# Kernel optimization log

Measured on AMD Instinct MI355X. Metric: run time of the kernel, lower is better.

## Reference

```python
import jax, jax.numpy as jnp
import numpy as np

NUM_HEADS = 16
ROPE_SEGMENTS = (1024, 512)  # remainder of the sequence is left un-roped
ROPE_THETA = 10000.0
EPS = 1e-6


def _rmsnorm(t, w):
    # t: [B,H,N,D]; norm over last dim in fp32, then scale
    tf = t.astype(jnp.float32)
    n = tf * jax.lax.rsqrt(jnp.mean(tf * tf, axis=-1, keepdims=True) + EPS)
    return n.astype(t.dtype) * w


def _rope(t):
    # t: [B,H,S,D]; positions restart at 0 for each call (segment-local RoPE)
    S, D = t.shape[-2], t.shape[-1]
    inv_freq = 1.0 / (ROPE_THETA ** (jnp.arange(0, D, 2, dtype=jnp.float32) / D))  # [D/2]
    ang = jnp.arange(S, dtype=jnp.float32)[:, None] * inv_freq[None, :]            # [S,D/2]
    cos, sin = jnp.cos(ang), jnp.sin(ang)
    t1, t2 = t[..., : D // 2], t[..., D // 2 :]
    return jnp.concatenate([t1 * cos - t2 * sin, t2 * cos + t1 * sin], axis=-1).astype(t.dtype)


def _segmented_rope(t, N):
    parts, start = [], 0
    for seg in ROPE_SEGMENTS:
        parts.append(_rope(t[:, :, start : start + seg, :]))
        start += seg
    if start < N:
        parts.append(t[:, :, start:, :])
    return jnp.concatenate(parts, axis=2)


def setup_inputs() -> dict:
    key = jax.random.key(0)
    ks = jax.random.split(key, 5)
    B, N, C = 2, 2048, 1024
    D = C // NUM_HEADS
    s = 1.0 / np.sqrt(C)
    return {
        "x": jax.random.normal(ks[0], (B, N, C), jnp.float32),
        "qkv_w": jax.random.normal(ks[1], (3 * C, C), jnp.float32) * s,
        "qkv_b": jax.random.normal(ks[2], (3 * C,), jnp.float32) * 0.02,
        "qn_w": jnp.ones((D,), jnp.float32),
        "kn_w": jnp.ones((D,), jnp.float32),
        "proj_w": jax.random.normal(ks[3], (C, C), jnp.float32) * s,
        "proj_b": jax.random.normal(ks[4], (C,), jnp.float32) * 0.02,
    }


def reference(x, qkv_w, qkv_b, qn_w, kn_w, proj_w, proj_b):
    B, N, C = x.shape
    H = NUM_HEADS
    D = C // H
    qkv = (x @ qkv_w.T + qkv_b).reshape(B, N, 3, H, D)
    qkv = jnp.transpose(qkv, (2, 0, 3, 1, 4))  # [3,B,H,N,D]
    q, k, v = qkv[0], qkv[1], qkv[2]
    q = _rmsnorm(q, qn_w)
    k = _rmsnorm(k, kn_w)
    q = _segmented_rope(q, N)
    k = _segmented_rope(k, N)
    scale = 1.0 / np.sqrt(D)  # SDPA default scale
    scores = jnp.einsum("bhqd,bhkd->bhqk", q, k) * scale
    attn = jax.nn.softmax(scores, axis=-1)
    out = jnp.einsum("bhqk,bhkd->bhqd", attn, v)           # [B,H,N,D]
    out = jnp.transpose(out, (0, 2, 1, 3)).reshape(B, N, C)
    return out @ proj_w.T + proj_b
```

## Files before the change

kernel.cpp:

```cpp
#include <hip/hip_runtime.h>

typedef __attribute__((ext_vector_type(8))) short short8;
typedef __attribute__((ext_vector_type(4))) float f32x4;

__device__ __forceinline__ float bf2f(unsigned short u) {
    union { unsigned int i; float f; } c; c.i = ((unsigned int)u) << 16; return c.f;
}
__device__ __forceinline__ unsigned short f2bf(float f) {
    union { float f; unsigned int i; } c; c.f = f;
    unsigned int u = c.i;
    return (unsigned short)((u + 0x7fffu + ((u >> 16) & 1u)) >> 16);
}

__device__ __forceinline__ void glds16(const void* g, void* l) {
    __builtin_amdgcn_global_load_lds(
        (const __attribute__((address_space(1))) unsigned int*)g,
        (__attribute__((address_space(3))) unsigned int*)l, 16, 0, 0);
}

__global__ __launch_bounds__(256) void prep(
    const float* __restrict__ x, const float* __restrict__ qkv_w,
    const float* __restrict__ proj_w,
    const float* __restrict__ qn_w, const float* __restrict__ kn_w,
    unsigned short* __restrict__ xb, unsigned short* __restrict__ qwb,
    unsigned short* __restrict__ pwb, float* __restrict__ mb2)
{
    const int b = blockIdx.x, tid = threadIdx.x;
    const float* src; unsigned short* dst; int i;
    if (b < 4096)      { src = x;      dst = xb;  i = b * 256 + tid; }
    else if (b < 7168) { src = qkv_w;  dst = qwb; i = (b - 4096) * 256 + tid; }
    else if (b < 8192) { src = proj_w; dst = pwb; i = (b - 7168) * 256 + tid; }
    else {
        if (tid < 64) {
            float a = fabsf(qn_w[tid]), bb = fabsf(kn_w[tid]);
#pragma unroll
            for (int off = 32; off; off >>= 1) {
                a = fmaxf(a, __shfl_xor(a, off));
                bb = fmaxf(bb, __shfl_xor(bb, off));
            }
            if (tid == 0) *mb2 = 8.0f * a * bb * 1.4426950408889634f;
        }
        return;
    }
    float4 v = ((const float4*)src)[i];
    ushort4 o;
    o.x = f2bf(v.x); o.y = f2bf(v.y); o.z = f2bf(v.z); o.w = f2bf(v.w);
    ((ushort4*)dst)[i] = o;
}

__global__ __launch_bounds__(256) void gemm_qkv(
    const unsigned short* __restrict__ A,
    const unsigned short* __restrict__ W,
    const float* __restrict__ bias,
    const float* __restrict__ qn_w, const float* __restrict__ kn_w,
    unsigned short* __restrict__ qb, unsigned short* __restrict__ kb,
    unsigned short* __restrict__ vt)
{
    __shared__ unsigned short As[128 * 32];
    __shared__ unsigned short Ws[128 * 32];
    const int tid = threadIdx.x;
    const int w = tid >> 6, l = tid & 63, quad = l >> 4, low = l & 15;
    const int m0 = blockIdx.y * 128, n0 = blockIdx.x * 128;
    const int wm = w >> 1, wn = w & 1;
    const int K = 1024;

    f32x4 acc[4][4];
#pragma unroll
    for (int i = 0; i < 4; i++)
#pragma unroll
        for (int j = 0; j < 4; j++) acc[i][j] = (f32x4){0.f, 0.f, 0.f, 0.f};

    const int r1 = tid >> 2, p1 = tid & 3;
    const int c1 = p1 ^ ((r1 >> 1) & 3);
    const int r2 = r1 + 64;
    const int c2 = p1 ^ ((r2 >> 1) & 3);
    const unsigned short* ga1 = A + (size_t)(m0 + r1) * K + c1 * 8;
    const unsigned short* ga2 = A + (size_t)(m0 + r2) * K + c2 * 8;
    const unsigned short* gw1 = W + (size_t)(n0 + r1) * K + c1 * 8;
    const unsigned short* gw2 = W + (size_t)(n0 + r2) * K + c2 * 8;
    char* lA = (char*)As + (w << 10);
    char* lW = (char*)Ws + (w << 10);

    for (int k0 = 0; k0 < K; k0 += 32) {
        __syncthreads();
        glds16(ga1 + k0, lA);
        glds16(ga2 + k0, lA + 4096);
        glds16(gw1 + k0, lW);
        glds16(gw2 + k0, lW + 4096);
        __syncthreads();
        short8 af[4], wf[4];
#pragma unroll
        for (int i = 0; i < 4; i++) {
            const int ra = wm * 64 + i * 16 + low;
            af[i] = *(const short8*)&As[ra * 32 + (quad ^ ((ra >> 1) & 3)) * 8];
            const int rw = wn * 64 + i * 16 + low;
            wf[i] = *(const short8*)&Ws[rw * 32 + (quad ^ ((rw >> 1) & 3)) * 8];
        }
#pragma unroll
        for (int i = 0; i < 4; i++)
#pragma unroll
            for (int j = 0; j < 4; j++)
                acc[i][j] = __builtin_amdgcn_mfma_f32_16x16x32_bf16(
                    af[i], wf[j], acc[i][j], 0, 0, 0);
    }

    const int colbase = n0 + wn * 64;
    const int t3 = colbase >> 10;
    const int hh = (colbase & 1023) >> 6;
    float wv4[4] = {0, 0, 0, 0}, invA = 0.f, invB = 0.f;
    if (t3 < 2) {
        const float* nw = (t3 == 0) ? qn_w : kn_w;
#pragma unroll
        for (int j = 0; j < 4; j++) wv4[j] = nw[j * 16 + low];
        const float c0 = -2.0f * 13.287712379549449f / 64.0f;
        invA = exp2f(c0 * (float)low);
        invB = exp2f(c0 * (float)(16 + low));
    }
    unsigned short* dqk = (t3 == 0) ? qb : kb;

#pragma unroll
    for (int i = 0; i < 4; i++) {
#pragma unroll
        for (int reg = 0; reg < 4; reg++) {
            const int gm = m0 + wm * 64 + i * 16 + quad * 4 + reg;
            const int b_ = gm >> 11, npos = gm & 2047;
            float v[4];
#pragma unroll
            for (int j = 0; j < 4; j++)
                v[j] = acc[i][j][reg] + bias[colbase + j * 16 + low];
            if (t3 == 2) {
#pragma unroll
                for (int j = 0; j < 4; j++)
                    vt[((size_t)(b_ * 16 + hh) * 64 + j * 16 + low) * 2048 + npos] =
                        f2bf(v[j]);
            } else {
                float ss = v[0]*v[0] + v[1]*v[1] + v[2]*v[2] + v[3]*v[3];
                ss += __shfl_xor(ss, 1); ss += __shfl_xor(ss, 2);
                ss += __shfl_xor(ss, 4); ss += __shfl_xor(ss, 8);
                const float r = rsqrtf(ss * (1.0f / 64.0f) + 1e-6f);
                float nv[4];
#pragma unroll
                for (int j = 0; j < 4; j++) nv[j] = v[j] * r * wv4[j];
                float o0, o1, o2, o3;
                if (npos < 1536) {
                    const float p = (float)((npos < 1024) ? npos : (npos - 1024));
                    float sA, cA, sB, cB;
                    __sincosf(p * invA, &sA, &cA);
                    __sincosf(p * invB, &sB, &cB);
                    o0 = nv[0] * cA - nv[2] * sA;
                    o1 = nv[1] * cB - nv[3] * sB;
                    o2 = nv[2] * cA + nv[0] * sA;
                    o3 = nv[3] * cB + nv[1] * sB;
                } else { o0 = nv[0]; o1 = nv[1]; o2 = nv[2]; o3 = nv[3]; }
                unsigned short* drow =
                    dqk + ((size_t)(b_ * 16 + hh) * 2048 + npos) * 64 + low;
                drow[0]  = f2bf(o0);
                drow[16] = f2bf(o1);
                drow[32] = f2bf(o2);
                drow[48] = f2bf(o3);
            }
        }
    }
}

__global__ __launch_bounds__(256) void flash_mfma(
    const unsigned short* __restrict__ qg, const unsigned short* __restrict__ kg,
    const unsigned short* __restrict__ vg, unsigned short* __restrict__ ao,
    const float* __restrict__ mb2p)
{
    __shared__ unsigned short Ks[64 * 64];
    __shared__ unsigned short Vs[64 * 64];
    __shared__ unsigned short Ps[4][16 * 72];

    const int tid = threadIdx.x;
    const int w = tid >> 6, l = tid & 63, quad = l >> 4, low = l & 15;
    const int bh = blockIdx.y, q0 = blockIdx.x * 64;
    const float MB2 = *mb2p;
    const float SCL = 0.125f * 1.4426950408889634f;

    short8 qa[2];
#pragma unroll
    for (int kh = 0; kh < 2; kh++) {
        const int qrow = q0 + w * 16 + low;
        qa[kh] = *(const short8*)(qg + ((size_t)bh * 2048 + qrow) * 64 +
                                  kh * 32 + quad * 8);
    }

    f32x4 o[4], lsum = (f32x4){0.f, 0.f, 0.f, 0.f};
#pragma unroll
    for (int db = 0; db < 4; db++) o[db] = (f32x4){0.f, 0.f, 0.f, 0.f};
    short8 ones;
#pragma unroll
    for (int j = 0; j < 8; j++) ones[j] = (short)0x3F80;

    const int kr1 = tid >> 3, kp1 = tid & 7, kc1 = kp1 ^ (kr1 & 7);
    const int kr2 = kr1 + 32, kc2 = kp1 ^ (kr2 & 7);
    const unsigned short* gk1 = kg + ((size_t)bh * 2048 + kr1) * 64 + kc1 * 8;
    const unsigned short* gk2 = kg + ((size_t)bh * 2048 + kr2) * 64 + kc2 * 8;
    const unsigned short* gv1 = vg + ((size_t)bh * 64 + kr1) * 2048 + kc1 * 8;
    const unsigned short* gv2 = vg + ((size_t)bh * 64 + kr2) * 2048 + kc2 * 8;
    char* lK = (char*)Ks + (w << 10);
    char* lV = (char*)Vs + (w << 10);
    unsigned short* myP = Ps[w];

    for (int kt = 0; kt < 32; kt++) {
        const size_t ko = (size_t)kt * 4096;
        const int vo = kt * 64;
        __syncthreads();
        glds16(gk1 + ko, lK);
        glds16(gk2 + ko, lK + 4096);
        glds16(gv1 + vo, lV);
        glds16(gv2 + vo, lV + 4096);
        __syncthreads();

#pragma unroll
        for (int kb = 0; kb < 4; kb++) {
            const int krow = kb * 16 + low;
            const short8 kf0 = *(const short8*)&Ks[krow * 64 + (quad ^ (krow & 7)) * 8];
            const short8 kf1 = *(const short8*)&Ks[krow * 64 + ((4 + quad) ^ (krow & 7)) * 8];
            f32x4 s = __builtin_amdgcn_mfma_f32_16x16x32_bf16(
                kf0, qa[0], (f32x4){0.f, 0.f, 0.f, 0.f}, 0, 0, 0);
            s = __builtin_amdgcn_mfma_f32_16x16x32_bf16(kf1, qa[1], s, 0, 0, 0);
            unsigned int pb[4];
#pragma unroll
            for (int reg = 0; reg < 4; reg++) {
                union { float f; unsigned int u; } cc;
                cc.f = exp2f(fmaf(s[reg], SCL, -MB2));
                pb[reg] = cc.u;
            }
            const unsigned int u0 = __builtin_amdgcn_perm(pb[1], pb[0], 0x07060302u);
            const unsigned int u1 = __builtin_amdgcn_perm(pb[3], pb[2], 0x07060302u);
            *(uint2*)&myP[low * 72 + kb * 16 + quad * 4] = make_uint2(u0, u1);
        }

        short8 pa[2];
#pragma unroll
        for (int kh = 0; kh < 2; kh++)
            pa[kh] = *(const short8*)&myP[low * 72 + kh * 32 + quad * 8];
        lsum = __builtin_amdgcn_mfma_f32_16x16x32_bf16(pa[0], ones, lsum, 0, 0, 0);
        lsum = __builtin_amdgcn_mfma_f32_16x16x32_bf16(pa[1], ones, lsum, 0, 0, 0);
#pragma unroll
        for (int db = 0; db < 4; db++) {
            const int d = db * 16 + low;
            const short8 vf0 = *(const short8*)&Vs[d * 64 + (quad ^ (d & 7)) * 8];
            const short8 vf1 = *(const short8*)&Vs[d * 64 + ((4 + quad) ^ (d & 7)) * 8];
            o[db] = __builtin_amdgcn_mfma_f32_16x16x32_bf16(pa[0], vf0, o[db], 0, 0, 0);
            o[db] = __builtin_amdgcn_mfma_f32_16x16x32_bf16(pa[1], vf1, o[db], 0, 0, 0);
        }
    }

    const int b_ = bh >> 4, h = bh & 15;
    float inv[4];
#pragma unroll
    for (int reg = 0; reg < 4; reg++) inv[reg] = 1.0f / lsum[reg];
#pragma unroll
    for (int db = 0; db < 4; db++)
#pragma unroll
        for (int reg = 0; reg < 4; reg++) {
            const int n = q0 + w * 16 + quad * 4 + reg;
            ao[((size_t)(b_ * 2048 + n)) * 1024 + h * 64 + db * 16 + low] =
                f2bf(o[db][reg] * inv[reg]);
        }
}

__global__ __launch_bounds__(256) void gemm_out(
    const unsigned short* __restrict__ A,
    const unsigned short* __restrict__ W,
    const float* __restrict__ bias,
    float* __restrict__ outp)
{
    __shared__ unsigned short As[64 * 32];
    __shared__ unsigned short Ws[128 * 32];
    const int tid = threadIdx.x;
    const int w = tid >> 6, l = tid & 63, quad = l >> 4, low = l & 15;
    const int m0 = blockIdx.y * 64, n0 = blockIdx.x * 128;
    const int wm = w >> 1, wn = w & 1;
    const int K = 1024;

    f32x4 acc[2][4];
#pragma unroll
    for (int i = 0; i < 2; i++)
#pragma unroll
        for (int j = 0; j < 4; j++) acc[i][j] = (f32x4){0.f, 0.f, 0.f, 0.f};

    const int r1 = tid >> 2, p1 = tid & 3;
    const int c1 = p1 ^ ((r1 >> 1) & 3);
    const int r2 = r1 + 64;
    const int c2 = p1 ^ ((r2 >> 1) & 3);
    const unsigned short* ga = A + (size_t)(m0 + r1) * K + c1 * 8;
    const unsigned short* gw1 = W + (size_t)(n0 + r1) * K + c1 * 8;
    const unsigned short* gw2 = W + (size_t)(n0 + r2) * K + c2 * 8;
    char* lA = (char*)As + (w << 10);
    char* lW = (char*)Ws + (w << 10);

    for (int k0 = 0; k0 < K; k0 += 32) {
        __syncthreads();
        glds16(ga + k0, lA);
        glds16(gw1 + k0, lW);
        glds16(gw2 + k0, lW + 4096);
        __syncthreads();
        short8 af[2], wf[4];
#pragma unroll
        for (int i = 0; i < 2; i++) {
            const int ra = wm * 32 + i * 16 + low;
            af[i] = *(const short8*)&As[ra * 32 + (quad ^ ((ra >> 1) & 3)) * 8];
        }
#pragma unroll
        for (int j = 0; j < 4; j++) {
            const int rw = wn * 64 + j * 16 + low;
            wf[j] = *(const short8*)&Ws[rw * 32 + (quad ^ ((rw >> 1) & 3)) * 8];
        }
#pragma unroll
        for (int i = 0; i < 2; i++)
#pragma unroll
            for (int j = 0; j < 4; j++)
                acc[i][j] = __builtin_amdgcn_mfma_f32_16x16x32_bf16(
                    af[i], wf[j], acc[i][j], 0, 0, 0);
    }

#pragma unroll
    for (int i = 0; i < 2; i++)
#pragma unroll
        for (int j = 0; j < 4; j++) {
            const int gc = n0 + wn * 64 + j * 16 + low;
            const float bv = bias[gc];
#pragma unroll
            for (int reg = 0; reg < 4; reg++) {
                const int gm = m0 + wm * 32 + i * 16 + quad * 4 + reg;
                outp[(size_t)gm * 1024 + gc] = acc[i][j][reg] + bv;
            }
        }
}

extern "C" void kernel_launch(void* const* d_in, const int* in_sizes, int n_in,
                              void* d_out, int out_size, void* d_ws, size_t ws_size,
                              hipStream_t stream)
{
    const float* x      = (const float*)d_in[0];
    const float* qkv_w  = (const float*)d_in[1];
    const float* qkv_b  = (const float*)d_in[2];
    const float* qn_w   = (const float*)d_in[3];
    const float* kn_w   = (const float*)d_in[4];
    const float* proj_w = (const float*)d_in[5];
    const float* proj_b = (const float*)d_in[6];

    char* base = (char*)d_ws;
    float* mb2          = (float*)base;
    unsigned short* xb  = (unsigned short*)(base + 256);
    unsigned short* qwb = xb  + 4194304;
    unsigned short* pwb = qwb + 3145728;
    unsigned short* qb  = pwb + 1048576;
    unsigned short* kb  = qb  + 4194304;
    unsigned short* vt  = kb  + 4194304;
    unsigned short* ao  = vt  + 4194304;

    prep<<<8193, 256, 0, stream>>>(x, qkv_w, proj_w, qn_w, kn_w, xb, qwb, pwb, mb2);

    gemm_qkv<<<dim3(24, 32), 256, 0, stream>>>(xb, qwb, qkv_b, qn_w, kn_w,
                                               qb, kb, vt);

    flash_mfma<<<dim3(32, 32), 256, 0, stream>>>(qb, kb, vt, ao, mb2);

    gemm_out<<<dim3(8, 64), 256, 0, stream>>>(ao, pwb, proj_b, (float*)d_out);
}
```

Before: 216.2 us.

## Use 32x32 MFMA in flash attention and stage V transpose through LDS

```diff
diff --git a/kernel.cpp b/kernel.cpp
--- a/kernel.cpp
+++ b/kernel.cpp
@@ -2,6 +2,7 @@
 
 typedef __attribute__((ext_vector_type(8))) short short8;
 typedef __attribute__((ext_vector_type(4))) float f32x4;
+typedef __attribute__((ext_vector_type(16))) float f32x16;
 
 __device__ __forceinline__ float bf2f(unsigned short u) {
     union { unsigned int i; float f; } c; c.i = ((unsigned int)u) << 16; return c.f;
@@ -17,6 +18,8 @@
         (const __attribute__((address_space(1))) unsigned int*)g,
         (__attribute__((address_space(3))) unsigned int*)l, 16, 0, 0);
 }
+
+union i4s8 { int4 i; short8 s; };
 
 __global__ __launch_bounds__(256) void prep(
     const float* __restrict__ x, const float* __restrict__ qkv_w,
@@ -56,8 +59,7 @@
     unsigned short* __restrict__ qb, unsigned short* __restrict__ kb,
     unsigned short* __restrict__ vt)
 {
-    __shared__ unsigned short As[128 * 32];
-    __shared__ unsigned short Ws[128 * 32];
+    __shared__ unsigned short pool[128 * 136];
     const int tid = threadIdx.x;
     const int w = tid >> 6, l = tid & 63, quad = l >> 4, low = l & 15;
     const int m0 = blockIdx.y * 128, n0 = blockIdx.x * 128;
@@ -78,8 +80,8 @@
     const unsigned short* ga2 = A + (size_t)(m0 + r2) * K + c2 * 8;
     const unsigned short* gw1 = W + (size_t)(n0 + r1) * K + c1 * 8;
     const unsigned short* gw2 = W + (size_t)(n0 + r2) * K + c2 * 8;
-    char* lA = (char*)As + (w << 10);
-    char* lW = (char*)Ws + (w << 10);
+    char* lA = (char*)pool + (w << 10);
+    char* lW = (char*)pool + 8192 + (w << 10);
 
     for (int k0 = 0; k0 < K; k0 += 32) {
         __syncthreads();
@@ -92,9 +94,9 @@
 #pragma unroll
         for (int i = 0; i < 4; i++) {
             const int ra = wm * 64 + i * 16 + low;
-            af[i] = *(const short8*)&As[ra * 32 + (quad ^ ((ra >> 1) & 3)) * 8];
+            af[i] = *(const short8*)&pool[ra * 32 + (quad ^ ((ra >> 1) & 3)) * 8];
             const int rw = wn * 64 + i * 16 + low;
-            wf[i] = *(const short8*)&Ws[rw * 32 + (quad ^ ((rw >> 1) & 3)) * 8];
+            wf[i] = *(const short8*)&pool[4096 + rw * 32 + (quad ^ ((rw >> 1) & 3)) * 8];
         }
 #pragma unroll
         for (int i = 0; i < 4; i++)
@@ -105,17 +107,44 @@
     }
 
     const int colbase = n0 + wn * 64;
-    const int t3 = colbase >> 10;
+    const int t3 = n0 >> 10;
     const int hh = (colbase & 1023) >> 6;
-    float wv4[4] = {0, 0, 0, 0}, invA = 0.f, invB = 0.f;
-    if (t3 < 2) {
-        const float* nw = (t3 == 0) ? qn_w : kn_w;
-#pragma unroll
-        for (int j = 0; j < 4; j++) wv4[j] = nw[j * 16 + low];
-        const float c0 = -2.0f * 13.287712379549449f / 64.0f;
-        invA = exp2f(c0 * (float)low);
-        invB = exp2f(c0 * (float)(16 + low));
-    }
+
+    if (t3 == 2) {
+        __syncthreads();
+#pragma unroll
+        for (int i = 0; i < 4; i++)
+#pragma unroll
+            for (int j = 0; j < 4; j++) {
+                const int c = wn * 64 + j * 16 + low;
+                const float bv = bias[n0 + c];
+#pragma unroll
+                for (int reg = 0; reg < 4; reg++) {
+                    const int r = wm * 64 + i * 16 + quad * 4 + reg;
+                    pool[c * 136 + r] = f2bf(acc[i][j][reg] + bv);
+                }
+            }
+        __syncthreads();
+        const int b_ = m0 >> 11, nbase = m0 & 2047;
+        const int rch = (tid & 15) * 8;
+#pragma unroll
+        for (int p = 0; p < 8; p++) {
+            const int c = (tid >> 4) + p * 16;
+            const int gc = n0 + c;
+            const int h2 = (gc & 1023) >> 6, d = gc & 63;
+            const short8 vv = *(const short8*)&pool[c * 136 + rch];
+            *(short8*)(vt + ((size_t)((b_ * 16 + h2) * 64 + d)) * 2048 + nbase + rch) = vv;
+        }
+        return;
+    }
+
+    const float* nw = (t3 == 0) ? qn_w : kn_w;
+    float wv4[4];
+#pragma unroll
+    for (int j = 0; j < 4; j++) wv4[j] = nw[j * 16 + low];
+    const float c0 = -2.0f * 13.287712379549449f / 64.0f;
+    const float invA = exp2f(c0 * (float)low);
+    const float invB = exp2f(c0 * (float)(16 + low));
     unsigned short* dqk = (t3 == 0) ? qb : kb;
 
 #pragma unroll
@@ -128,37 +157,30 @@
 #pragma unroll
             for (int j = 0; j < 4; j++)
                 v[j] = acc[i][j][reg] + bias[colbase + j * 16 + low];
-            if (t3 == 2) {
-#pragma unroll
-                for (int j = 0; j < 4; j++)
-                    vt[((size_t)(b_ * 16 + hh) * 64 + j * 16 + low) * 2048 + npos] =
-                        f2bf(v[j]);
-            } else {
-                float ss = v[0]*v[0] + v[1]*v[1] + v[2]*v[2] + v[3]*v[3];
-                ss += __shfl_xor(ss, 1); ss += __shfl_xor(ss, 2);
-                ss += __shfl_xor(ss, 4); ss += __shfl_xor(ss, 8);
-                const float r = rsqrtf(ss * (1.0f / 64.0f) + 1e-6f);
-                float nv[4];
-#pragma unroll
-                for (int j = 0; j < 4; j++) nv[j] = v[j] * r * wv4[j];
-                float o0, o1, o2, o3;
-                if (npos < 1536) {
-                    const float p = (float)((npos < 1024) ? npos : (npos - 1024));
-                    float sA, cA, sB, cB;
-                    __sincosf(p * invA, &sA, &cA);
-                    __sincosf(p * invB, &sB, &cB);
-                    o0 = nv[0] * cA - nv[2] * sA;
-                    o1 = nv[1] * cB - nv[3] * sB;
-                    o2 = nv[2] * cA + nv[0] * sA;
-                    o3 = nv[3] * cB + nv[1] * sB;
-                } else { o0 = nv[0]; o1 = nv[1]; o2 = nv[2]; o3 = nv[3]; }
-                unsigned short* drow =
-                    dqk + ((size_t)(b_ * 16 + hh) * 2048 + npos) * 64 + low;
-                drow[0]  = f2bf(o0);
-                drow[16] = f2bf(o1);
-                drow[32] = f2bf(o2);
-                drow[48] = f2bf(o3);
-            }
+            float ss = v[0]*v[0] + v[1]*v[1] + v[2]*v[2] + v[3]*v[3];
+            ss += __shfl_xor(ss, 1); ss += __shfl_xor(ss, 2);
+            ss += __shfl_xor(ss, 4); ss += __shfl_xor(ss, 8);
+            const float r = rsqrtf(ss * (1.0f / 64.0f) + 1e-6f);
+            float nv[4];
+#pragma unroll
+            for (int j = 0; j < 4; j++) nv[j] = v[j] * r * wv4[j];
+            float o0, o1, o2, o3;
+            if (npos < 1536) {
+                const float p = (float)((npos < 1024) ? npos : (npos - 1024));
+                float sA, cA, sB, cB;
+                __sincosf(p * invA, &sA, &cA);
+                __sincosf(p * invB, &sB, &cB);
+                o0 = nv[0] * cA - nv[2] * sA;
+                o1 = nv[1] * cB - nv[3] * sB;
+                o2 = nv[2] * cA + nv[0] * sA;
+                o3 = nv[3] * cB + nv[1] * sB;
+            } else { o0 = nv[0]; o1 = nv[1]; o2 = nv[2]; o3 = nv[3]; }
+            unsigned short* drow =
+                dqk + ((size_t)(b_ * 16 + hh) * 2048 + npos) * 64 + low;
+            drow[0]  = f2bf(o0);
+            drow[16] = f2bf(o1);
+            drow[32] = f2bf(o2);
+            drow[48] = f2bf(o3);
         }
     }
 }
@@ -170,28 +192,25 @@
 {
     __shared__ unsigned short Ks[64 * 64];
     __shared__ unsigned short Vs[64 * 64];
-    __shared__ unsigned short Ps[4][16 * 72];
 
     const int tid = threadIdx.x;
-    const int w = tid >> 6, l = tid & 63, quad = l >> 4, low = l & 15;
-    const int bh = blockIdx.y, q0 = blockIdx.x * 64;
+    const int w = tid >> 6, lane = tid & 63, h5 = lane >> 5, l5 = lane & 31;
+    const int bh = blockIdx.y, q0 = blockIdx.x * 128;
     const float MB2 = *mb2p;
     const float SCL = 0.125f * 1.4426950408889634f;
 
-    short8 qa[2];
-#pragma unroll
-    for (int kh = 0; kh < 2; kh++) {
-        const int qrow = q0 + w * 16 + low;
-        qa[kh] = *(const short8*)(qg + ((size_t)bh * 2048 + qrow) * 64 +
-                                  kh * 32 + quad * 8);
-    }
-
-    f32x4 o[4], lsum = (f32x4){0.f, 0.f, 0.f, 0.f};
-#pragma unroll
-    for (int db = 0; db < 4; db++) o[db] = (f32x4){0.f, 0.f, 0.f, 0.f};
-    short8 ones;
-#pragma unroll
-    for (int j = 0; j < 8; j++) ones[j] = (short)0x3F80;
+    short8 qf[4];
+    {
+        const unsigned short* qrow = qg + ((size_t)bh * 2048 + q0 + w * 32 + l5) * 64;
+#pragma unroll
+        for (int ks = 0; ks < 4; ks++)
+            qf[ks] = *(const short8*)(qrow + ks * 16 + h5 * 8);
+    }
+
+    f32x16 o0, o1, ls;
+#pragma unroll
+    for (int i = 0; i < 16; i++) { o0[i] = 0.f; o1[i] = 0.f; ls[i] = 0.f; }
+    i4s8 ones; ones.i = make_int4(0x3F803F80, 0x3F803F80, 0x3F803F80, 0x3F803F80);
 
     const int kr1 = tid >> 3, kp1 = tid & 7, kc1 = kp1 ^ (kr1 & 7);
     const int kr2 = kr1 + 32, kc2 = kp1 ^ (kr2 & 7);
@@ -201,7 +220,6 @@
     const unsigned short* gv2 = vg + ((size_t)bh * 64 + kr2) * 2048 + kc2 * 8;
     char* lK = (char*)Ks + (w << 10);
     char* lV = (char*)Vs + (w << 10);
-    unsigned short* myP = Ps[w];
 
     for (int kt = 0; kt < 32; kt++) {
         const size_t ko = (size_t)kt * 4096;
@@ -214,53 +232,64 @@
         __syncthreads();
 
 #pragma unroll
-        for (int kb = 0; kb < 4; kb++) {
-            const int krow = kb * 16 + low;
-            const short8 kf0 = *(const short8*)&Ks[krow * 64 + (quad ^ (krow & 7)) * 8];
-            const short8 kf1 = *(const short8*)&Ks[krow * 64 + ((4 + quad) ^ (krow & 7)) * 8];
-            f32x4 s = __builtin_amdgcn_mfma_f32_16x16x32_bf16(
-                kf0, qa[0], (f32x4){0.f, 0.f, 0.f, 0.f}, 0, 0, 0);
-            s = __builtin_amdgcn_mfma_f32_16x16x32_bf16(kf1, qa[1], s, 0, 0, 0);
-            unsigned int pb[4];
-#pragma unroll
-            for (int reg = 0; reg < 4; reg++) {
-                union { float f; unsigned int u; } cc;
-                cc.f = exp2f(fmaf(s[reg], SCL, -MB2));
-                pb[reg] = cc.u;
-            }
-            const unsigned int u0 = __builtin_amdgcn_perm(pb[1], pb[0], 0x07060302u);
-            const unsigned int u1 = __builtin_amdgcn_perm(pb[3], pb[2], 0x07060302u);
-            *(uint2*)&myP[low * 72 + kb * 16 + quad * 4] = make_uint2(u0, u1);
-        }
-
-        short8 pa[2];
-#pragma unroll
-        for (int kh = 0; kh < 2; kh++)
-            pa[kh] = *(const short8*)&myP[low * 72 + kh * 32 + quad * 8];
-        lsum = __builtin_amdgcn_mfma_f32_16x16x32_bf16(pa[0], ones, lsum, 0, 0, 0);
-        lsum = __builtin_amdgcn_mfma_f32_16x16x32_bf16(pa[1], ones, lsum, 0, 0, 0);
-#pragma unroll
-        for (int db = 0; db < 4; db++) {
-            const int d = db * 16 + low;
-            const short8 vf0 = *(const short8*)&Vs[d * 64 + (quad ^ (d & 7)) * 8];
-            const short8 vf1 = *(const short8*)&Vs[d * 64 + ((4 + quad) ^ (d & 7)) * 8];
-            o[db] = __builtin_amdgcn_mfma_f32_16x16x32_bf16(pa[0], vf0, o[db], 0, 0, 0);
-            o[db] = __builtin_amdgcn_mfma_f32_16x16x32_bf16(pa[1], vf1, o[db], 0, 0, 0);
+        for (int kbk = 0; kbk < 2; kbk++) {
+            f32x16 s;
+#pragma unroll
+            for (int i = 0; i < 16; i++) s[i] = 0.f;
+            const int krow = kbk * 32 + l5;
+#pragma unroll
+            for (int ks = 0; ks < 4; ks++) {
+                const int ch = (h5 + 2 * ks) ^ (krow & 7);
+                const short8 kf = *(const short8*)&Ks[krow * 64 + ch * 8];
+                s = __builtin_amdgcn_mfma_f32_32x32x16_bf16(kf, qf[ks], s, 0, 0, 0);
+            }
+            unsigned int dw[8], pdw[8];
+#pragma unroll
+            for (int r = 0; r < 8; r++) {
+                union { float f; unsigned int u; } a, b;
+                a.f = exp2f(fmaf(s[2 * r],     SCL, -MB2));
+                b.f = exp2f(fmaf(s[2 * r + 1], SCL, -MB2));
+                dw[r] = __builtin_amdgcn_perm(b.u, a.u, 0x07060302u);
+            }
+#pragma unroll
+            for (int r = 0; r < 8; r++) pdw[r] = __shfl_xor((int)dw[r], 32);
+            i4s8 f0, f1;
+            f0.i.x = h5 ? pdw[2] : dw[0];
+            f0.i.y = h5 ? pdw[3] : dw[1];
+            f0.i.z = h5 ? dw[2]  : pdw[0];
+            f0.i.w = h5 ? dw[3]  : pdw[1];
+            f1.i.x = h5 ? pdw[6] : dw[4];
+            f1.i.y = h5 ? pdw[7] : dw[5];
+            f1.i.z = h5 ? dw[6]  : pdw[4];
+            f1.i.w = h5 ? dw[7]  : pdw[5];
+
+            ls = __builtin_amdgcn_mfma_f32_32x32x16_bf16(f0.s, ones.s, ls, 0, 0, 0);
+            ls = __builtin_amdgcn_mfma_f32_32x32x16_bf16(f1.s, ones.s, ls, 0, 0, 0);
+
+#pragma unroll
+            for (int nb = 0; nb < 2; nb++) {
+                const int vrow = nb * 32 + l5;
+                const int chb = kbk * 4 + h5;
+                const short8 vfa = *(const short8*)&Vs[vrow * 64 + ((chb    ) ^ (vrow & 7)) * 8];
+                const short8 vfb = *(const short8*)&Vs[vrow * 64 + ((chb + 2) ^ (vrow & 7)) * 8];
+                f32x16& oo = nb ? o1 : o0;
+                oo = __builtin_amdgcn_mfma_f32_32x32x16_bf16(f0.s, vfa, oo, 0, 0, 0);
+                oo = __builtin_amdgcn_mfma_f32_32x32x16_bf16(f1.s, vfb, oo, 0, 0, 0);
+            }
         }
     }
 
     const int b_ = bh >> 4, h = bh & 15;
-    float inv[4];
-#pragma unroll
-    for (int reg = 0; reg < 4; reg++) inv[reg] = 1.0f / lsum[reg];
-#pragma unroll
-    for (int db = 0; db < 4; db++)
-#pragma unroll
-        for (int reg = 0; reg < 4; reg++) {
-            const int n = q0 + w * 16 + quad * 4 + reg;
-            ao[((size_t)(b_ * 2048 + n)) * 1024 + h * 64 + db * 16 + low] =
-                f2bf(o[db][reg] * inv[reg]);
-        }
+    float inv[16];
+#pragma unroll
+    for (int r = 0; r < 16; r++) inv[r] = 1.0f / ls[r];
+#pragma unroll
+    for (int r = 0; r < 16; r++) {
+        const int n = q0 + w * 32 + (r & 3) + 8 * (r >> 2) + 4 * h5;
+        const size_t rowb = ((size_t)(b_ * 2048 + n)) * 1024 + h * 64;
+        ao[rowb + l5]      = f2bf(o0[r] * inv[r]);
+        ao[rowb + 32 + l5] = f2bf(o1[r] * inv[r]);
+    }
 }
 
 __global__ __launch_bounds__(256) void gemm_out(
@@ -359,7 +388,7 @@
     gemm_qkv<<<dim3(24, 32), 256, 0, stream>>>(xb, qwb, qkv_b, qn_w, kn_w,
                                                qb, kb, vt);
 
-    flash_mfma<<<dim3(32, 32), 256, 0, stream>>>(qb, kb, vt, ao, mb2);
+    flash_mfma<<<dim3(16, 32), 256, 0, stream>>>(qb, kb, vt, ao, mb2);
 
     gemm_out<<<dim3(8, 64), 256, 0, stream>>>(ao, pwb, proj_b, (float*)d_out);
 }
```

Result: slower. 221.5 us (+2.5%).
